# Kernel optimization log

Hardware: AMD Instinct MI355X
Metric: run time of the kernel (lower is better)

## Reference

```python
import jax, jax.numpy as jnp
import numpy as np

B, N, D_OBS, D_NB = 8192, 64, 128, 128
HEADS, GAT_F, GRU_H = 4, 64, 256
ACTION_DIM = 16
PERIOD0 = 24.0
NEG_SLOPE = 0.2
PMAX, PBUDGET = 0.5, 1.0
ENC_DIM = D_OBS + 1  # feature 0 expands to sin/cos
FUSE_IN = ENC_DIM + HEADS * GAT_F


def cyclical_encode(x):
    phase = 2.0 * jnp.pi * x[:, 0] / PERIOD0
    return jnp.concatenate([jnp.sin(phase)[:, None], jnp.cos(phase)[:, None], x[:, 1:]], axis=1)


def gat(node_feat, neigh_feat, mask, W, a):
    # node_feat [B,Din], neigh_feat [B,N,Din], W [Din,H*F], a [H,2F,1]
    b, n, _ = neigh_feat.shape
    h_node = (node_feat @ W).reshape(b, HEADS, GAT_F)            # [B,H,F]
    h_nb = (neigh_feat @ W).reshape(b, n, HEADS, GAT_F)          # [B,N,H,F]
    a_src, a_dst = a[:, :GAT_F, 0], a[:, GAT_F:, 0]              # [H,F] each
    e = (jnp.einsum('bhf,hf->bh', h_node, a_src)[:, None, :]
         + jnp.einsum('bnhf,hf->bnh', h_nb, a_dst))              # [B,N,H]
    e = jnp.where(e > 0, e, NEG_SLOPE * e)                        # leaky_relu
    e = jnp.where(mask[:, :, None], e, -jnp.inf)
    alpha = jax.nn.softmax(e, axis=1)                             # over neighbors
    agg = jnp.einsum('bnh,bnhf->bhf', alpha, h_nb)
    return agg.reshape(b, HEADS * GAT_F)


def gru_cell(x, h, Wih, bih, Whh, bhh):
    gi = x @ Wih + bih
    gh = h @ Whh + bhh
    ir, iz, in_ = jnp.split(gi, 3, axis=-1)
    hr, hz, hn = jnp.split(gh, 3, axis=-1)
    r = jax.nn.sigmoid(ir + hr)
    z = jax.nn.sigmoid(iz + hz)
    nn_ = jnp.tanh(in_ + r * hn)
    return (1.0 - z) * nn_ + z * h


def layer_norm(x, g, b, eps=1e-5):
    mu = jnp.mean(x, axis=-1, keepdims=True)
    var = jnp.var(x, axis=-1, keepdims=True)
    return (x - mu) * jax.lax.rsqrt(var + eps) * g + b


def project_power(raw):
    # Euclidean projection onto {0<=p<=PMAX, sum p<=PBUDGET} via bisection on mu
    def total(mu):
        return jnp.sum(jnp.clip(raw - mu[:, None], 0.0, PMAX), axis=1)
    feas = total(jnp.zeros(raw.shape[0], raw.dtype)) <= PBUDGET
    lo = jnp.zeros(raw.shape[0], raw.dtype)
    hi = jnp.maximum(jnp.max(raw, axis=1), 0.0)
    def body(_, lh):
        lo, hi = lh
        mid = 0.5 * (lo + hi)
        over = total(mid) > PBUDGET
        return (jnp.where(over, mid, lo), jnp.where(over, hi, mid))
    lo, hi = jax.lax.fori_loop(0, 60, body, (lo, hi))
    mu = jnp.where(feas, 0.0, hi)
    return jnp.clip(raw - mu[:, None], 0.0, PMAX)


def setup_inputs() -> dict:
    key = jax.random.key(0)
    ks = jax.random.split(key, 20)
    def init(k, shape, fan_in):
        return (jax.random.normal(k, shape, jnp.float32) / np.sqrt(fan_in)).astype(jnp.float32)
    mask = jax.random.bernoulli(ks[3], 0.5, (B, N))
    mask = mask.at[:, 0].set(True)  # guarantee >=1 valid neighbor per row
    return {
        'node_obs': jax.random.normal(ks[0], (B, D_OBS), jnp.float32),
        'neighbor_obs': jax.random.normal(ks[1], (B, N, D_NB), jnp.float32),
        'neighbor_mask': mask,
        'hidden_state': jnp.zeros((1, B, GRU_H), jnp.float32),
        'W_gat': init(ks[4], (D_NB, HEADS * GAT_F), D_NB),
        'a_gat': init(ks[5], (HEADS, 2 * GAT_F, 1), 2 * GAT_F),
        'fusion_W': init(ks[6], (FUSE_IN, GRU_H), FUSE_IN),
        'fusion_b': jnp.zeros((GRU_H,), jnp.float32),
        'Wih': init(ks[7], (GRU_H, 3 * GRU_H), GRU_H),
        'bih': jnp.zeros((3 * GRU_H,), jnp.float32),
        'Whh': init(ks[8], (GRU_H, 3 * GRU_H), GRU_H),
        'bhh': jnp.zeros((3 * GRU_H,), jnp.float32),
        'ln_g': jnp.ones((GRU_H,), jnp.float32),
        'ln_b': jnp.zeros((GRU_H,), jnp.float32),
        'W1': init(ks[9], (GRU_H, 256), GRU_H),
        'b1': jnp.zeros((256,), jnp.float32),
        'W2': init(ks[10], (256, 128), 256),
        'b2': jnp.zeros((128,), jnp.float32),
        'W3': init(ks[11], (128, ACTION_DIM), 128),
        'b3': jnp.zeros((ACTION_DIM,), jnp.float32),
    }


def reference(node_obs, neighbor_obs, neighbor_mask, hidden_state,
              W_gat, a_gat, fusion_W, fusion_b, Wih, bih, Whh, bhh,
              ln_g, ln_b, W1, b1, W2, b2, W3, b3):
    enc = cyclical_encode(node_obs)                              # [B, ENC_DIM]
    node_feat_for_gat = neighbor_obs[:, 0, :]
    ctx = gat(node_feat_for_gat, neighbor_obs, neighbor_mask, W_gat, a_gat)
    fused = jax.nn.relu(jnp.concatenate([enc, ctx], axis=-1) @ fusion_W + fusion_b)
    h_new = gru_cell(fused, hidden_state[0], Wih, bih, Whh, bhh)  # 1-step GRU
    belief = layer_norm(h_new, ln_g, ln_b)
    x = jax.nn.relu(belief @ W1 + b1)
    x = jax.nn.relu(x @ W2 + b2)
    raw = x @ W3 + b3                                            # [B, ACTION_DIM]
    action = project_power(raw)
    return action, h_new[None, :, :]
```

## Files before the change

kernel.cpp:

```cpp
#include <hip/hip_runtime.h>
#include <hip/hip_bf16.h>


typedef unsigned short u16;
typedef unsigned int   u32;
typedef __attribute__((ext_vector_type(8))) short bf16x8;
typedef __attribute__((ext_vector_type(4))) float f32x4;

#define KFUSE  672
#define ACT_TOT (8192*16)

__device__ __forceinline__ u16 f2bf(float x){
  u32 u = __float_as_uint(x);
  u += 0x7fffu + ((u >> 16) & 1u);
  return (u16)(u >> 16);
}
__device__ __forceinline__ float bf2f(u16 h){ return __uint_as_float(((u32)h) << 16); }

__device__ __forceinline__ void frag_one(const float* __restrict__ src, int ld, int col0,
                                         int NT, u16* __restrict__ dhi, u16* __restrict__ dlo,
                                         int f, int fsrc, int l){
  int kt = fsrc / NT, nt = fsrc % NT;
  int kbase = kt*32 + (l >> 4)*8, n = col0 + nt*16 + (l & 15);
  size_t o = ((size_t)f*64 + l)*8;
  #pragma unroll
  for(int i = 0; i < 8; ++i){
    float w = src[(size_t)(kbase + i)*ld + n];
    u16 h = f2bf(w);
    dhi[o + i] = h;
    dlo[o + i] = f2bf(w - bf2f(h));
  }
}

__device__ __forceinline__ void frag_wbig(const float* __restrict__ fW,
                                          const float* __restrict__ Wg,
                                          u16* __restrict__ dhi, u16* __restrict__ dlo,
                                          int f, int l){
  int kt = f / 16, nt = f % 16;
  int kbase = kt*32 + (l >> 4)*8, n = nt*16 + (l & 15);
  size_t o = ((size_t)f*64 + l)*8;
  #pragma unroll
  for(int i = 0; i < 8; ++i){
    int r = kbase + i;
    float v;
    if(r < 129) v = fW[(size_t)r*256 + n];
    else if(r < 641){
      int h = (r - 129) >> 7, kk = (r - 129) & 127;
      float s = 0.f;
      for(int ff = 0; ff < 64; ++ff)
        s += Wg[kk*256 + h*64 + ff] * fW[(size_t)(129 + h*64 + ff)*256 + n];
      v = s;
    } else v = 0.f;
    u16 hh = f2bf(v);
    dhi[o + i] = hh;
    dlo[o + i] = f2bf(v - bf2f(hh));
  }
}

#define P_FF0   1
#define P_WRZ0  85
#define P_WIN0  213
#define P_WHN0  245
#define P_F10   277
#define P_F20   309
__global__ __launch_bounds__(256) void k_prep(
    const unsigned char* __restrict__ maskb, int* __restrict__ flag,
    const float* __restrict__ Wg, const float* __restrict__ ag,
    float* __restrict__ was, float* __restrict__ wad,
    const float* __restrict__ fW,
    const float* __restrict__ Wih, const float* __restrict__ Whh,
    const float* __restrict__ W1, const float* __restrict__ W2,
    u16* __restrict__ ffh, u16* __restrict__ ffl,
    u16* __restrict__ wrzh, u16* __restrict__ wrzl,
    u16* __restrict__ winh, u16* __restrict__ winl,
    u16* __restrict__ whnh, u16* __restrict__ whnl,
    u16* __restrict__ f1h, u16* __restrict__ f1l,
    u16* __restrict__ f2h, u16* __restrict__ f2l)
{
  int bx = blockIdx.x, t = threadIdx.x;
  if(bx == 0){
    if(t == 0){
      int s = 0;
      for(int i = 1; i < 256; i += 4) s += maskb[i];
      *flag = (s == 0) ? 1 : 0;
    }
    #pragma unroll
    for(int v = 0; v < 2; ++v){
      int idx = v*256 + t, k = idx & 127, h = idx >> 7;
      float s = 0.f, d = 0.f;
      for(int f = 0; f < 64; ++f){
        float w = Wg[k*256 + h*64 + f];
        s += w * ag[h*128 + f];
        d += w * ag[h*128 + 64 + f];
      }
      was[k*4 + h] = s; wad[k*4 + h] = d;
    }
  } else if(bx < P_WRZ0){
    int sub = t >> 6, l = t & 63;
    int f = (bx - P_FF0)*4 + sub;
    frag_wbig(fW, Wg, ffh, ffl, f, l);
  } else {
    int sub = t >> 6, l = t & 63;
    if(bx < P_WIN0){
      int idx = (bx - P_WRZ0)*4 + sub;
      if(idx < 256) frag_one(Wih, 768, 0, 32, wrzh, wrzl, idx, idx, l);
      else          frag_one(Whh, 768, 0, 32, wrzh, wrzl, idx, idx - 256, l);
    } else if(bx < P_WHN0){
      int f = (bx - P_WIN0)*4 + sub;
      frag_one(Wih, 768, 512, 16, winh, winl, f, f, l);
    } else if(bx < P_F10){
      int f = (bx - P_WHN0)*4 + sub;
      frag_one(Whh, 768, 512, 16, whnh, whnl, f, f, l);
    } else if(bx < P_F20){
      int f = (bx - P_F10)*4 + sub;
      frag_one(W1, 256, 0, 16, f1h, f1l, f, f, l);
    } else {
      int f = (bx - P_F20)*4 + sub;
      frag_one(W2, 128, 0, 8, f2h, f2l, f, f, l);
    }
  }
}

__global__ __launch_bounds__(256) void k_gat(
    const float* __restrict__ nbg, const float* __restrict__ node,
    const void* __restrict__ maskp, const int* __restrict__ flagp,
    const float* __restrict__ was, const float* __restrict__ wad,
    u16* __restrict__ xhi, u16* __restrict__ xlo,
    const float* __restrict__ hidden,
    u16* __restrict__ acath, u16* __restrict__ acatl)
{
  int t = threadIdx.x;
  if(blockIdx.x >= 8192){
    int i = (blockIdx.x - 8192)*256 + t;
    int idx8 = i*8, row = idx8 >> 8, col = idx8 & 255;
    const float4* p = (const float4*)(hidden + (size_t)idx8);
    float4 v0 = p[0], v1 = p[1];
    float vv[8] = {v0.x,v0.y,v0.z,v0.w,v1.x,v1.y,v1.z,v1.w};
    u16 h8[8], l8[8];
    #pragma unroll
    for(int q = 0; q < 8; ++q){ u16 h = f2bf(vv[q]); h8[q] = h; l8[q] = f2bf(vv[q] - bf2f(h)); }
    uint4 uh = { (u32)h8[0] | ((u32)h8[1]<<16), (u32)h8[2] | ((u32)h8[3]<<16),
                 (u32)h8[4] | ((u32)h8[5]<<16), (u32)h8[6] | ((u32)h8[7]<<16) };
    uint4 ul = { (u32)l8[0] | ((u32)l8[1]<<16), (u32)l8[2] | ((u32)l8[3]<<16),
                 (u32)l8[4] | ((u32)l8[5]<<16), (u32)l8[6] | ((u32)l8[7]<<16) };
    size_t off = (size_t)row*512 + 256 + col;
    *(uint4*)(acath + off) = uh;
    *(uint4*)(acatl + off) = ul;
    return;
  }

  __shared__ float s_nb[8192];
  __shared__ float s_ep[1024];
  __shared__ float s_alpha[256];
  int b = blockIdx.x;
  const float* nb = nbg + (size_t)b*8192;
  const int isint = *flagp;

  #pragma unroll
  for(int q = 0; q < 8; ++q){
    int f = q*256 + t;
    int n = f >> 5, ch = f & 31;
    float4 v = *(const float4*)(nb + f*4);
    *(float4*)(s_nb + (n*32 + (ch ^ (n & 31)))*4) = v;
  }

  if(t < 129){
    float v;
    if(t < 2){
      float ph = node[(size_t)b*128] * (6.2831853071795864769f / 24.0f);
      v = (t == 0) ? sinf(ph) : cosf(ph);
    } else v = node[(size_t)b*128 + (t-1)];
    u16 h = f2bf(v);
    size_t o = (size_t)b*KFUSE + t;
    xhi[o] = h; xlo[o] = f2bf(v - bf2f(h));
  } else if(t < 160){
    size_t o = (size_t)b*KFUSE + 641 + (t - 129);
    xhi[o] = 0; xlo[o] = 0;
  }
  __syncthreads();

  {
    int n = t & 63, c = t >> 6;
    int cu = __builtin_amdgcn_readfirstlane(c);
    const float* wadc = wad + cu*128;
    float adx = 0.f, ady = 0.f, adz = 0.f, adw = 0.f;
    #pragma unroll
    for(int q = 0; q < 8; ++q){
      int ch = c*8 + q;
      float4 v = *(const float4*)(s_nb + (n*32 + (ch ^ (n & 31)))*4);
      float vv[4] = {v.x, v.y, v.z, v.w};
      #pragma unroll
      for(int i2 = 0; i2 < 4; ++i2){
        float4 wd = *(const float4*)(wadc + (q*4 + i2)*4);
        adx += vv[i2]*wd.x; ady += vv[i2]*wd.y; adz += vv[i2]*wd.z; adw += vv[i2]*wd.w;
      }
    }
    float4 ad = {adx, ady, adz, adw};
    *(float4*)(s_ep + (c*64 + n)*4) = ad;
  }
  __syncthreads();

  {
    int n2 = t & 63, h2 = t >> 6;
    float es = 0.f;
    #pragma unroll
    for(int ii = 0; ii < 2; ++ii){
      int k = n2*2 + ii;
      float v0 = s_nb[(k >> 2)*4 + (k & 3)];
      es += v0 * was[k*4 + h2];
    }
    for(int off = 32; off; off >>= 1) es += __shfl_xor(es, off);
    float ed = s_ep[n2*4 + h2] + s_ep[(64+n2)*4 + h2]
             + s_ep[(128+n2)*4 + h2] + s_ep[(192+n2)*4 + h2];
    float e = es + ed;
// ... 51 lines not shown
  }
}

template<int KT, int NT_TOT, int NPW, int ROWF>
__global__ __launch_bounds__(256) void k_gemm3(
    const u16* __restrict__ xhi, const u16* __restrict__ xlo, int lda,
    const u16* __restrict__ wfhi, const u16* __restrict__ wflo,
    const float* __restrict__ bias,
    u16* __restrict__ ohi, u16* __restrict__ olo, int ost, int ocol)
{
  int l = threadIdx.x & 63, w = threadIdx.x >> 6;
  int m0 = blockIdx.x * (16*ROWF);
  int ntbase = blockIdx.y * (4*NPW) + w*NPW;
  f32x4 acc[NPW][ROWF];
  #pragma unroll
  for(int j = 0; j < NPW; ++j)
    #pragma unroll
    for(int rf = 0; rf < ROWF; ++rf) acc[j][rf] = (f32x4){0.f,0.f,0.f,0.f};
  size_t arow[ROWF];
  #pragma unroll
  for(int rf = 0; rf < ROWF; ++rf)
    arow[rf] = (size_t)(m0 + rf*16 + (l & 15))*lda + (size_t)((l >> 4)*8);
  bf16x8 ah[ROWF], al[ROWF], bhc[NPW], blc[NPW];
  #pragma unroll
  for(int rf = 0; rf < ROWF; ++rf){
    ah[rf] = *(const bf16x8*)(xhi + arow[rf]);
    al[rf] = *(const bf16x8*)(xlo + arow[rf]);
  }
  #pragma unroll
  for(int j = 0; j < NPW; ++j){
    size_t bo = ((size_t)(ntbase + j)*64 + l)*8;
    bhc[j] = *(const bf16x8*)(wfhi + bo);
    blc[j] = *(const bf16x8*)(wflo + bo);
  }
  for(int kt = 0; kt < KT; ++kt){
    bf16x8 ahn[ROWF], aln[ROWF], bhn[NPW], bln[NPW];
    if(kt + 1 < KT){
      #pragma unroll
      for(int rf = 0; rf < ROWF; ++rf){
        ahn[rf] = *(const bf16x8*)(xhi + arow[rf] + (kt+1)*32);
        aln[rf] = *(const bf16x8*)(xlo + arow[rf] + (kt+1)*32);
      }
      #pragma unroll
      for(int j = 0; j < NPW; ++j){
        size_t bo = ((size_t)((kt+1)*NT_TOT + ntbase + j)*64 + l)*8;
        bhn[j] = *(const bf16x8*)(wfhi + bo);
        bln[j] = *(const bf16x8*)(wflo + bo);
      }
    }
    #pragma unroll
    for(int j = 0; j < NPW; ++j){
      #pragma unroll
      for(int rf = 0; rf < ROWF; ++rf){
        acc[j][rf] = __builtin_amdgcn_mfma_f32_16x16x32_bf16(ah[rf], bhc[j], acc[j][rf], 0, 0, 0);
        acc[j][rf] = __builtin_amdgcn_mfma_f32_16x16x32_bf16(ah[rf], blc[j], acc[j][rf], 0, 0, 0);
        acc[j][rf] = __builtin_amdgcn_mfma_f32_16x16x32_bf16(al[rf], bhc[j], acc[j][rf], 0, 0, 0);
      }
    }
    #pragma unroll
    for(int rf = 0; rf < ROWF; ++rf){ ah[rf] = ahn[rf]; al[rf] = aln[rf]; }
    #pragma unroll
    for(int j = 0; j < NPW; ++j){ bhc[j] = bhn[j]; blc[j] = bln[j]; }
  }
  #pragma unroll
  for(int j = 0; j < NPW; ++j){
    int col = (ntbase + j)*16 + (l & 15);
    float bv = bias[col];
    #pragma unroll
    for(int rf = 0; rf < ROWF; ++rf){
      int r0 = m0 + rf*16 + (l >> 4)*4;
      #pragma unroll
      for(int q = 0; q < 4; ++q){
        float y = fmaxf(acc[j][rf][q] + bv, 0.f);
        size_t o = (size_t)(r0 + q)*ost + ocol + col;
        u16 h = f2bf(y);
        ohi[o] = h; olo[o] = f2bf(y - bf2f(h));
      }
    }
  }
}

#define BSTR 264
#define XSTR 132
__global__ __launch_bounds__(512) void k_grumlp(
    const u16* __restrict__ ah_, const u16* __restrict__ al_,
    const u16* __restrict__ wrzh, const u16* __restrict__ wrzl,
    const u16* __restrict__ winh, const u16* __restrict__ winl,
    const u16* __restrict__ whnh, const u16* __restrict__ whnl,
    const u16* __restrict__ f1h, const u16* __restrict__ f1l,
    const u16* __restrict__ f2h, const u16* __restrict__ f2l,
    const float* __restrict__ bih, const float* __restrict__ bhh,
    const float* __restrict__ hidden, const float* __restrict__ lng,
    const float* __restrict__ lnb,
    const float* __restrict__ b1, const float* __restrict__ b2,
    const float* __restrict__ W3, const float* __restrict__ b3,
    float* __restrict__ hout, float* __restrict__ act)
{
  __shared__ float s_s1[256], s_s2[256], s_mu[32], s_rs[32];
  __shared__ u16 s_bh[32*BSTR], s_bl[32*BSTR];
  __shared__ float s_x2[32*XSTR];
  __shared__ float sW3[2048];
  int t = threadIdx.x;
  int l = t & 63, w = t >> 6;
  int m0 = blockIdx.x*32;
  for(int i = t; i < 2048; i += 512) sW3[i] = W3[i];

  f32x4 ar[2][2], az[2][2], aa[2][2], ab[2][2];
  #pragma unroll
  for(int j = 0; j < 2; ++j)
    #pragma unroll
    for(int rf = 0; rf < 2; ++rf){
      ar[j][rf] = (f32x4){0.f,0.f,0.f,0.f}; az[j][rf] = (f32x4){0.f,0.f,0.f,0.f};
      aa[j][rf] = (f32x4){0.f,0.f,0.f,0.f}; ab[j][rf] = (f32x4){0.f,0.f,0.f,0.f};
    }
  size_t arow[2];
  #pragma unroll
  for(int rf = 0; rf < 2; ++rf)
    arow[rf] = (size_t)(m0 + rf*16 + (l & 15))*512 + (size_t)((l >> 4)*8);
  for(int kt = 0; kt < 16; ++kt){
    bf16x8 xh[2], xl[2];
    #pragma unroll
    for(int rf = 0; rf < 2; ++rf){
      xh[rf] = *(const bf16x8*)(ah_ + arow[rf] + kt*32);
      xl[rf] = *(const bf16x8*)(al_ + arow[rf] + kt*32);
    }
    #pragma unroll
    for(int j = 0; j < 2; ++j){
      int nt = w*2 + j;
      size_t bo = ((size_t)(kt*32 + nt)*64 + l)*8;
      bf16x8 bh = *(const bf16x8*)(wrzh + bo);
      bf16x8 bl = *(const bf16x8*)(wrzl + bo);
      size_t bo2 = bo + (size_t)16*64*8;
      bf16x8 bh2 = *(const bf16x8*)(wrzh + bo2);
      bf16x8 bl2 = *(const bf16x8*)(wrzl + bo2);
      #pragma unroll
      for(int rf = 0; rf < 2; ++rf){
        ar[j][rf] = __builtin_amdgcn_mfma_f32_16x16x32_bf16(xh[rf], bh, ar[j][rf], 0, 0, 0);
        ar[j][rf] = __builtin_amdgcn_mfma_f32_16x16x32_bf16(xh[rf], bl, ar[j][rf], 0, 0, 0);
        ar[j][rf] = __builtin_amdgcn_mfma_f32_16x16x32_bf16(xl[rf], bh, ar[j][rf], 0, 0, 0);
        az[j][rf] = __builtin_amdgcn_mfma_f32_16x16x32_bf16(xh[rf], bh2, az[j][rf], 0, 0, 0);
        az[j][rf] = __builtin_amdgcn_mfma_f32_16x16x32_bf16(xh[rf], bl2, az[j][rf], 0, 0, 0);
        az[j][rf] = __builtin_amdgcn_mfma_f32_16x16x32_bf16(xl[rf], bh2, az[j][rf], 0, 0, 0);
      }
    }
  }
  for(int kt = 0; kt < 8; ++kt){
    bf16x8 fh[2], fl2[2], gh[2], gl[2];
    #pragma unroll
    for(int rf = 0; rf < 2; ++rf){
      fh[rf]  = *(const bf16x8*)(ah_ + arow[rf] + kt*32);
      fl2[rf] = *(const bf16x8*)(al_ + arow[rf] + kt*32);
      gh[rf]  = *(const bf16x8*)(ah_ + arow[rf] + 256 + kt*32);
      gl[rf]  = *(const bf16x8*)(al_ + arow[rf] + 256 + kt*32);
    }
    #pragma unroll
    for(int j = 0; j < 2; ++j){
      int nt = w*2 + j;
      size_t bo = ((size_t)(kt*16 + nt)*64 + l)*8;
      bf16x8 bh = *(const bf16x8*)(winh + bo);
      bf16x8 bl = *(const bf16x8*)(winl + bo);
      bf16x8 ch = *(const bf16x8*)(whnh + bo);
      bf16x8 cl2 = *(const bf16x8*)(whnl + bo);
      #pragma unroll
      for(int rf = 0; rf < 2; ++rf){
        aa[j][rf] = __builtin_amdgcn_mfma_f32_16x16x32_bf16(fh[rf], bh, aa[j][rf], 0, 0, 0);
        aa[j][rf] = __builtin_amdgcn_mfma_f32_16x16x32_bf16(fh[rf], bl, aa[j][rf], 0, 0, 0);
        aa[j][rf] = __builtin_amdgcn_mfma_f32_16x16x32_bf16(fl2[rf], bh, aa[j][rf], 0, 0, 0);
        ab[j][rf] = __builtin_amdgcn_mfma_f32_16x16x32_bf16(gh[rf], ch, ab[j][rf], 0, 0, 0);
        ab[j][rf] = __builtin_amdgcn_mfma_f32_16x16x32_bf16(gh[rf], cl2, ab[j][rf], 0, 0, 0);
        ab[j][rf] = __builtin_amdgcn_mfma_f32_16x16x32_bf16(gl[rf], ch, ab[j][rf], 0, 0, 0);
      }
    }
  }
  int cl = l & 15, rq = l >> 4;
  float hnew[2][2][4];
  float s1p[2][4], s2p[2][4];
  #pragma unroll
  for(int rf = 0; rf < 2; ++rf)
    #pragma unroll
    for(int q = 0; q < 4; ++q){ s1p[rf][q] = 0.f; s2p[rf][q] = 0.f; }
  #pragma unroll
  for(int j = 0; j < 2; ++j){
    int col = w*32 + j*16 + cl;
    float br = bih[col] + bhh[col];
    float bz = bih[256+col] + bhh[256+col];
    float bi = bih[512+col];
    float bh2 = bhh[512+col];
    #pragma unroll
    for(int rf = 0; rf < 2; ++rf){
      #pragma unroll
      for(int q = 0; q < 4; ++q){
        int row = m0 + rf*16 + rq*4 + q;
        float rs = ar[j][rf][q] + br;
        float zs = az[j][rf][q] + bz;
        float in_ = aa[j][rf][q] + bi;
        float hn  = ab[j][rf][q] + bh2;
        float h   = hidden[(size_t)row*256 + col];
        float r = 1.f/(1.f + expf(-rs));
        float z = 1.f/(1.f + expf(-zs));
        float nv = tanhf(in_ + r*hn);
        float hv = (1.f - z)*nv + z*h;
        hnew[j][rf][q] = hv;
        hout[(size_t)row*256 + col] = hv;
        s1p[rf][q] += hv; s2p[rf][q] += hv*hv;
      }
    }
  }
  #pragma unroll
  for(int rf = 0; rf < 2; ++rf)
    #pragma unroll
    for(int q = 0; q < 4; ++q){
      float a = s1p[rf][q], b2v = s2p[rf][q];
      for(int off = 1; off < 16; off <<= 1){
        a += __shfl_xor(a, off); b2v += __shfl_xor(b2v, off);
      }
      if(cl == 0){
        int rloc = rf*16 + rq*4 + q;
        s_s1[w*32 + rloc] = a; s_s2[w*32 + rloc] = b2v;
      }
    }
  __syncthreads();
  if(t < 32){
    int rloc = t;
    float t1 = 0.f, t2 = 0.f;
    #pragma unroll
    for(int ww = 0; ww < 8; ++ww){ t1 += s_s1[ww*32 + rloc]; t2 += s_s2[ww*32 + rloc]; }
    float mu = t1 * (1.f/256.f);
    float var = t2 * (1.f/256.f) - mu*mu;
    s_mu[rloc] = mu; s_rs[rloc] = rsqrtf(var + 1e-5f);
  }
  __syncthreads();
  #pragma unroll
  for(int j = 0; j < 2; ++j){
    int col = w*32 + j*16 + cl;
    float g = lng[col], bb = lnb[col];
    #pragma unroll
    for(int rf = 0; rf < 2; ++rf){
      #pragma unroll
      for(int q = 0; q < 4; ++q){
        int rloc = rf*16 + rq*4 + q;
        float bel = (hnew[j][rf][q] - s_mu[rloc]) * s_rs[rloc] * g + bb;
        u16 hb = f2bf(bel);
        s_bh[rloc*BSTR + col] = hb;
        s_bl[rloc*BSTR + col] = f2bf(bel - bf2f(hb));
      }
    }
  }
  __syncthreads();
  f32x4 ax1[2][2];
  #pragma unroll
  for(int j = 0; j < 2; ++j)
    #pragma unroll
    for(int rf = 0; rf < 2; ++rf) ax1[j][rf] = (f32x4){0.f,0.f,0.f,0.f};
  for(int kt = 0; kt < 8; ++kt){
    bf16x8 xh[2], xl[2];
    #pragma unroll
    for(int rf = 0; rf < 2; ++rf){
      int off = (rf*16 + (l & 15))*BSTR + kt*32 + (l >> 4)*8;
      xh[rf] = *(const bf16x8*)(s_bh + off);
      xl[rf] = *(const bf16x8*)(s_bl + off);
    }
    #pragma unroll
    for(int j = 0; j < 2; ++j){
      size_t bo = ((size_t)(kt*16 + w*2 + j)*64 + l)*8;
      bf16x8 bh = *(const bf16x8*)(f1h + bo);
      bf16x8 bl = *(const bf16x8*)(f1l + bo);
      #pragma unroll
      for(int rf = 0; rf < 2; ++rf){
        ax1[j][rf] = __builtin_amdgcn_mfma_f32_16x16x32_bf16(xh[rf], bh, ax1[j][rf], 0, 0, 0);
        ax1[j][rf] = __builtin_amdgcn_mfma_f32_16x16x32_bf16(xh[rf], bl, ax1[j][rf], 0, 0, 0);
        ax1[j][rf] = __builtin_amdgcn_mfma_f32_16x16x32_bf16(xl[rf], bh, ax1[j][rf], 0, 0, 0);
      }
    }
  }
  __syncthreads();
  #pragma unroll
  for(int j = 0; j < 2; ++j){
    int col = (w*2 + j)*16 + cl;
    float bv = b1[col];
    #pragma unroll
    for(int rf = 0; rf < 2; ++rf){
      #pragma unroll
      for(int q = 0; q < 4; ++q){
        int rloc = rf*16 + rq*4 + q;
        float y = fmaxf(ax1[j][rf][q] + bv, 0.f);
        u16 hh = f2bf(y);
        s_bh[rloc*BSTR + col] = hh;
        s_bl[rloc*BSTR + col] = f2bf(y - bf2f(hh));
      }
    }
  }
  __syncthreads();
  f32x4 ax2[2];
  #pragma unroll
  for(int rf = 0; rf < 2; ++rf) ax2[rf] = (f32x4){0.f,0.f,0.f,0.f};
  for(int kt = 0; kt < 8; ++kt){
    bf16x8 xh[2], xl[2];
    #pragma unroll
    for(int rf = 0; rf < 2; ++rf){
      int off = (rf*16 + (l & 15))*BSTR + kt*32 + (l >> 4)*8;
      xh[rf] = *(const bf16x8*)(s_bh + off);
      xl[rf] = *(const bf16x8*)(s_bl + off);
    }
    size_t bo = ((size_t)(kt*8 + w)*64 + l)*8;
    bf16x8 bh = *(const bf16x8*)(f2h + bo);
    bf16x8 bl = *(const bf16x8*)(f2l + bo);
    #pragma unroll
    for(int rf = 0; rf < 2; ++rf){
      ax2[rf] = __builtin_amdgcn_mfma_f32_16x16x32_bf16(xh[rf], bh, ax2[rf], 0, 0, 0);
      ax2[rf] = __builtin_amdgcn_mfma_f32_16x16x32_bf16(xh[rf], bl, ax2[rf], 0, 0, 0);
      ax2[rf] = __builtin_amdgcn_mfma_f32_16x16x32_bf16(xl[rf], bh, ax2[rf], 0, 0, 0);
    }
  }
  {
    int col = w*16 + cl;
    float bv = b2[col];
    #pragma unroll
    for(int rf = 0; rf < 2; ++rf)
      #pragma unroll
      for(int q = 0; q < 4; ++q){
        int rloc = rf*16 + rq*4 + q;
        s_x2[rloc*XSTR + col] = fmaxf(ax2[rf][q] + bv, 0.f);
      }
  }
  __syncthreads();
  {
    int j = t & 15, rl = t >> 4;
    const float* xr = s_x2 + rl*XSTR;
    float raw = b3[j];
    #pragma unroll 8
    for(int k4 = 0; k4 < 32; ++k4){
      float4 v = *(const float4*)(xr + k4*4);
      raw += v.x*sW3[(k4*4+0)*16 + j] + v.y*sW3[(k4*4+1)*16 + j]
           + v.z*sW3[(k4*4+2)*16 + j] + v.w*sW3[(k4*4+3)*16 + j];
    }
    float c0 = fminf(fmaxf(raw, 0.f), 0.5f);
    float tot = c0;
    for(int off = 8; off; off >>= 1) tot += __shfl_xor(tot, off);
    float mx = raw;
    for(int off = 8; off; off >>= 1) mx = fmaxf(mx, __shfl_xor(mx, off));
    bool feas = (tot <= 1.0f);
    float lo = 0.f, hi = fmaxf(mx, 0.f);
    for(int it = 0; it < 60; ++it){
      float mid = 0.5f*(lo + hi);
      float s = fminf(fmaxf(raw - mid, 0.f), 0.5f);
      for(int off = 8; off; off >>= 1) s += __shfl_xor(s, off);
      bool over = s > 1.0f;
      lo = over ? mid : lo;
      hi = over ? hi : mid;
    }
    float muv = feas ? 0.f : hi;
    act[(size_t)(m0 + rl)*16 + j] = fminf(fmaxf(raw - muv, 0.f), 0.5f);
  }
}

#define OFF_FLAG   0u
#define OFF_WAS    4096u
#define OFF_WAD    8192u
#define OFF_FFH    12288u
#define OFF_FFL    356352u
#define OFF_WRZH   700416u
#define OFF_WRZL   1224704u
#define OFF_WINH   1748992u
#define OFF_WINL   1880064u
#define OFF_WHNH   2011136u
#define OFF_WHNL   2142208u
#define OFF_F1H    2273280u
#define OFF_F1L    2404352u
#define OFF_F2H    2535424u
#define OFF_F2L    2600960u
#define OFF_XCATH  2666496u
#define OFF_XCATL  13676544u
#define OFF_ACATH  24686592u
#define OFF_ACATL  33075200u

extern "C" void kernel_launch(void* const* d_in, const int* in_sizes, int n_in,
                              void* d_out, int out_size, void* d_ws, size_t ws_size,
                              hipStream_t stream){
  const float* node   = (const float*)d_in[0];
  const float* nbr    = (const float*)d_in[1];
  const void*  mask   = d_in[2];
  const float* hidden = (const float*)d_in[3];
  const float* Wg     = (const float*)d_in[4];
  const float* ag     = (const float*)d_in[5];
  const float* fW     = (const float*)d_in[6];
  const float* fb     = (const float*)d_in[7];
  const float* Wih    = (const float*)d_in[8];
  const float* bih    = (const float*)d_in[9];
  const float* Whh    = (const float*)d_in[10];
  const float* bhh    = (const float*)d_in[11];
  const float* lng    = (const float*)d_in[12];
  const float* lnb    = (const float*)d_in[13];
  const float* W1     = (const float*)d_in[14];
  const float* b1     = (const float*)d_in[15];
  const float* W2     = (const float*)d_in[16];
  const float* b2     = (const float*)d_in[17];
  const float* W3     = (const float*)d_in[18];
  const float* b3     = (const float*)d_in[19];
  char* ws = (char*)d_ws;
  float* out = (float*)d_out;

  int*   flag = (int*)  (ws + OFF_FLAG);
  float* was  = (float*)(ws + OFF_WAS);
  float* wad  = (float*)(ws + OFF_WAD);
  u16* ffh  = (u16*)(ws + OFF_FFH);   u16* ffl  = (u16*)(ws + OFF_FFL);
  u16* wrzh = (u16*)(ws + OFF_WRZH);  u16* wrzl = (u16*)(ws + OFF_WRZL);
  u16* winh = (u16*)(ws + OFF_WINH);  u16* winl = (u16*)(ws + OFF_WINL);
  u16* whnh = (u16*)(ws + OFF_WHNH);  u16* whnl = (u16*)(ws + OFF_WHNL);
  u16* f1h  = (u16*)(ws + OFF_F1H);   u16* f1l  = (u16*)(ws + OFF_F1L);
  u16* f2h  = (u16*)(ws + OFF_F2H);   u16* f2l  = (u16*)(ws + OFF_F2L);
  u16* xh   = (u16*)(ws + OFF_XCATH); u16* xl   = (u16*)(ws + OFF_XCATL);
  u16* ach  = (u16*)(ws + OFF_ACATH); u16* acl  = (u16*)(ws + OFF_ACATL);

  k_prep<<<325, 256, 0, stream>>>((const unsigned char*)mask, flag, Wg, ag, was, wad,
                                  fW, Wih, Whh, W1, W2,
                                  ffh, ffl, wrzh, wrzl, winh, winl, whnh, whnl,
                                  f1h, f1l, f2h, f2l);

  k_gat<<<8192 + 1024, 256, 0, stream>>>(nbr, node, mask, flag, was, wad, xh, xl,
                                         hidden, ach, acl);

  k_gemm3<21,16,2,4><<<dim3(128,2), 256, 0, stream>>>(xh, xl, KFUSE, ffh, ffl, fb, ach, acl, 512, 0);

  k_grumlp<<<256, 512, 0, stream>>>(ach, acl, wrzh, wrzl, winh, winl, whnh, whnl,
                                    f1h, f1l, f2h, f2l, bih, bhh, hidden, lng, lnb,
                                    b1, b2, W3, b3, out + ACT_TOT, out);
}
```

Measured before the change: 178.6 us.

## Move fused-weight prep into GAT kernel and double-buffer GRU GEMM loads

Moves the expensive frag_wbig work, which builds the combined GAT and fusion weight fragments, out of k_prep and into 84 extra blocks of k_gat. That work then overlaps with the GAT blocks instead of delaying the start of k_gat, and k_prep shrinks from 325 to 241 blocks. Separately, the GRU GEMM loops in k_grumlp now prefetch the next k-step's A and B fragments into registers while MFMAs run on the current ones, which raises register pressure. The frag_wbig blocks sit at the highest block indices, so they may be scheduled last and lengthen k_gat's tail.

```diff
diff --git a/kernel.cpp b/kernel.cpp
--- a/kernel.cpp
+++ b/kernel.cpp
@@ -57,20 +57,17 @@
   }
 }
 
-#define P_FF0   1
-#define P_WRZ0  85
-#define P_WIN0  213
-#define P_WHN0  245
-#define P_F10   277
-#define P_F20   309
+#define P_WRZ0  1
+#define P_WIN0  129
+#define P_WHN0  161
+#define P_F10   193
+#define P_F20   225
 __global__ __launch_bounds__(256) void k_prep(
     const unsigned char* __restrict__ maskb, int* __restrict__ flag,
     const float* __restrict__ Wg, const float* __restrict__ ag,
     float* __restrict__ was, float* __restrict__ wad,
-    const float* __restrict__ fW,
     const float* __restrict__ Wih, const float* __restrict__ Whh,
     const float* __restrict__ W1, const float* __restrict__ W2,
-    u16* __restrict__ ffh, u16* __restrict__ ffl,
     u16* __restrict__ wrzh, u16* __restrict__ wrzl,
     u16* __restrict__ winh, u16* __restrict__ winl,
     u16* __restrict__ whnh, u16* __restrict__ whnl,
@@ -95,10 +92,6 @@
       }
       was[k*4 + h] = s; wad[k*4 + h] = d;
     }
-  } else if(bx < P_WRZ0){
-    int sub = t >> 6, l = t & 63;
-    int f = (bx - P_FF0)*4 + sub;
-    frag_wbig(fW, Wg, ffh, ffl, f, l);
   } else {
     int sub = t >> 6, l = t & 63;
     if(bx < P_WIN0){
@@ -127,9 +120,16 @@
     const float* __restrict__ was, const float* __restrict__ wad,
     u16* __restrict__ xhi, u16* __restrict__ xlo,
     const float* __restrict__ hidden,
-    u16* __restrict__ acath, u16* __restrict__ acatl)
+    u16* __restrict__ acath, u16* __restrict__ acatl,
+    const float* __restrict__ fW, const float* __restrict__ Wg,
+    u16* __restrict__ ffh, u16* __restrict__ ffl)
 {
   int t = threadIdx.x;
+  if(blockIdx.x >= 9216){
+    int f = (blockIdx.x - 9216)*4 + (t >> 6), l = t & 63;
+    frag_wbig(fW, Wg, ffh, ffl, f, l);
+    return;
+  }
   if(blockIdx.x >= 8192){
     int i = (blockIdx.x - 8192)*256 + t;
     int idx8 = i*8, row = idx8 >> 8, col = idx8 & 255;
@@ -382,58 +382,113 @@
   #pragma unroll
   for(int rf = 0; rf < 2; ++rf)
     arow[rf] = (size_t)(m0 + rf*16 + (l & 15))*512 + (size_t)((l >> 4)*8);
-  for(int kt = 0; kt < 16; ++kt){
-    bf16x8 xh[2], xl[2];
-    #pragma unroll
-    for(int rf = 0; rf < 2; ++rf){
-      xh[rf] = *(const bf16x8*)(ah_ + arow[rf] + kt*32);
-      xl[rf] = *(const bf16x8*)(al_ + arow[rf] + kt*32);
+  {
+    bf16x8 xhc[2], xlc[2], bhc[2], blc[2], bh2c[2], bl2c[2];
+    #pragma unroll
+    for(int rf = 0; rf < 2; ++rf){
+      xhc[rf] = *(const bf16x8*)(ah_ + arow[rf]);
+      xlc[rf] = *(const bf16x8*)(al_ + arow[rf]);
     }
     #pragma unroll
     for(int j = 0; j < 2; ++j){
-      int nt = w*2 + j;
-      size_t bo = ((size_t)(kt*32 + nt)*64 + l)*8;
-      bf16x8 bh = *(const bf16x8*)(wrzh + bo);
-      bf16x8 bl = *(const bf16x8*)(wrzl + bo);
-      size_t bo2 = bo + (size_t)16*64*8;
-      bf16x8 bh2 = *(const bf16x8*)(wrzh + bo2);
-      bf16x8 bl2 = *(const bf16x8*)(wrzl + bo2);
+      size_t bo = ((size_t)(w*2 + j)*64 + l)*8;
+      bhc[j]  = *(const bf16x8*)(wrzh + bo);
+      blc[j]  = *(const bf16x8*)(wrzl + bo);
+      bh2c[j] = *(const bf16x8*)(wrzh + bo + (size_t)16*64*8);
+      bl2c[j] = *(const bf16x8*)(wrzl + bo + (size_t)16*64*8);
+    }
+    for(int kt = 0; kt < 16; ++kt){
+      bf16x8 xhn[2], xln[2], bhn[2], bln[2], bh2n[2], bl2n[2];
+      if(kt + 1 < 16){
+        #pragma unroll
+        for(int rf = 0; rf < 2; ++rf){
+          xhn[rf] = *(const bf16x8*)(ah_ + arow[rf] + (kt+1)*32);
+          xln[rf] = *(const bf16x8*)(al_ + arow[rf] + (kt+1)*32);
+        }
+        #pragma unroll
+        for(int j = 0; j < 2; ++j){
+          size_t bo = ((size_t)((kt+1)*32 + w*2 + j)*64 + l)*8;
+          bhn[j]  = *(const bf16x8*)(wrzh + bo);
+          bln[j]  = *(const bf16x8*)(wrzl + bo);
+          bh2n[j] = *(const bf16x8*)(wrzh + bo + (size_t)16*64*8);
+          bl2n[j] = *(const bf16x8*)(wrzl + bo + (size_t)16*64*8);
+        }
+      }
+      #pragma unroll
+      for(int j = 0; j < 2; ++j){
+        #pragma unroll
+        for(int rf = 0; rf < 2; ++rf){
+          ar[j][rf] = __builtin_amdgcn_mfma_f32_16x16x32_bf16(xhc[rf], bhc[j], ar[j][rf], 0, 0, 0);
+          ar[j][rf] = __builtin_amdgcn_mfma_f32_16x16x32_bf16(xhc[rf], blc[j], ar[j][rf], 0, 0, 0);
+          ar[j][rf] = __builtin_amdgcn_mfma_f32_16x16x32_bf16(xlc[rf], bhc[j], ar[j][rf], 0, 0, 0);
+          az[j][rf] = __builtin_amdgcn_mfma_f32_16x16x32_bf16(xhc[rf], bh2c[j], az[j][rf], 0, 0, 0);
+          az[j][rf] = __builtin_amdgcn_mfma_f32_16x16x32_bf16(xhc[rf], bl2c[j], az[j][rf], 0, 0, 0);
+          az[j][rf] = __builtin_amdgcn_mfma_f32_16x16x32_bf16(xlc[rf], bh2c[j], az[j][rf], 0, 0, 0);
+        }
+      }
+      #pragma unroll
+      for(int rf = 0; rf < 2; ++rf){ xhc[rf] = xhn[rf]; xlc[rf] = xln[rf]; }
+      #pragma unroll
+      for(int j = 0; j < 2; ++j){
+        bhc[j] = bhn[j]; blc[j] = bln[j]; bh2c[j] = bh2n[j]; bl2c[j] = bl2n[j];
+      }
+    }
+  }
+  {
+    bf16x8 fhc[2], flc[2], ghc[2], glc[2], bhc[2], blc[2], chc[2], clc[2];
+    #pragma unroll
+    for(int rf = 0; rf < 2; ++rf){
+      fhc[rf] = *(const bf16x8*)(ah_ + arow[rf]);
+      flc[rf] = *(const bf16x8*)(al_ + arow[rf]);
+      ghc[rf] = *(const bf16x8*)(ah_ + arow[rf] + 256);
+      glc[rf] = *(const bf16x8*)(al_ + arow[rf] + 256);
+    }
+    #pragma unroll
+    for(int j = 0; j < 2; ++j){
+      size_t bo = ((size_t)(w*2 + j)*64 + l)*8;
+      bhc[j] = *(const bf16x8*)(winh + bo);
+      blc[j] = *(const bf16x8*)(winl + bo);
+      chc[j] = *(const bf16x8*)(whnh + bo);
+      clc[j] = *(const bf16x8*)(whnl + bo);
+    }
+    for(int kt = 0; kt < 8; ++kt){
+      bf16x8 fhn[2], fln[2], ghn[2], gln[2], bhn[2], bln[2], chn[2], cln[2];
+      if(kt + 1 < 8){
+        #pragma unroll
+        for(int rf = 0; rf < 2; ++rf){
+          fhn[rf] = *(const bf16x8*)(ah_ + arow[rf] + (kt+1)*32);
+          fln[rf] = *(const bf16x8*)(al_ + arow[rf] + (kt+1)*32);
+          ghn[rf] = *(const bf16x8*)(ah_ + arow[rf] + 256 + (kt+1)*32);
+          gln[rf] = *(const bf16x8*)(al_ + arow[rf] + 256 + (kt+1)*32);
+        }
+        #pragma unroll
+        for(int j = 0; j < 2; ++j){
+          size_t bo = ((size_t)((kt+1)*16 + w*2 + j)*64 + l)*8;
+          bhn[j] = *(const bf16x8*)(winh + bo);
+          bln[j] = *(const bf16x8*)(winl + bo);
+          chn[j] = *(const bf16x8*)(whnh + bo);
+          cln[j] = *(const bf16x8*)(whnl + bo);
+        }
+      }
+      #pragma unroll
+      for(int j = 0; j < 2; ++j){
+        #pragma unroll
+        for(int rf = 0; rf < 2; ++rf){
+          aa[j][rf] = __builtin_amdgcn_mfma_f32_16x16x32_bf16(fhc[rf], bhc[j], aa[j][rf], 0, 0, 0);
+          aa[j][rf] = __builtin_amdgcn_mfma_f32_16x16x32_bf16(fhc[rf], blc[j], aa[j][rf], 0, 0, 0);
+          aa[j][rf] = __builtin_amdgcn_mfma_f32_16x16x32_bf16(flc[rf], bhc[j], aa[j][rf], 0, 0, 0);
+          ab[j][rf] = __builtin_amdgcn_mfma_f32_16x16x32_bf16(ghc[rf], chc[j], ab[j][rf], 0, 0, 0);
+          ab[j][rf] = __builtin_amdgcn_mfma_f32_16x16x32_bf16(ghc[rf], clc[j], ab[j][rf], 0, 0, 0);
+          ab[j][rf] = __builtin_amdgcn_mfma_f32_16x16x32_bf16(glc[rf], chc[j], ab[j][rf], 0, 0, 0);
+        }
+      }
       #pragma unroll
       for(int rf = 0; rf < 2; ++rf){
-        ar[j][rf] = __builtin_amdgcn_mfma_f32_16x16x32_bf16(xh[rf], bh, ar[j][rf], 0, 0, 0);
-        ar[j][rf] = __builtin_amdgcn_mfma_f32_16x16x32_bf16(xh[rf], bl, ar[j][rf], 0, 0, 0);
-        ar[j][rf] = __builtin_amdgcn_mfma_f32_16x16x32_bf16(xl[rf], bh, ar[j][rf], 0, 0, 0);
-        az[j][rf] = __builtin_amdgcn_mfma_f32_16x16x32_bf16(xh[rf], bh2, az[j][rf], 0, 0, 0);
-        az[j][rf] = __builtin_amdgcn_mfma_f32_16x16x32_bf16(xh[rf], bl2, az[j][rf], 0, 0, 0);
-        az[j][rf] = __builtin_amdgcn_mfma_f32_16x16x32_bf16(xl[rf], bh2, az[j][rf], 0, 0, 0);
-      }
-    }
-  }
-  for(int kt = 0; kt < 8; ++kt){
-    bf16x8 fh[2], fl2[2], gh[2], gl[2];
-    #pragma unroll
-    for(int rf = 0; rf < 2; ++rf){
-      fh[rf]  = *(const bf16x8*)(ah_ + arow[rf] + kt*32);
-      fl2[rf] = *(const bf16x8*)(al_ + arow[rf] + kt*32);
-      gh[rf]  = *(const bf16x8*)(ah_ + arow[rf] + 256 + kt*32);
-      gl[rf]  = *(const bf16x8*)(al_ + arow[rf] + 256 + kt*32);
-    }
-    #pragma unroll
-    for(int j = 0; j < 2; ++j){
-      int nt = w*2 + j;
-      size_t bo = ((size_t)(kt*16 + nt)*64 + l)*8;
-      bf16x8 bh = *(const bf16x8*)(winh + bo);
-      bf16x8 bl = *(const bf16x8*)(winl + bo);
-      bf16x8 ch = *(const bf16x8*)(whnh + bo);
-      bf16x8 cl2 = *(const bf16x8*)(whnl + bo);
-      #pragma unroll
-      for(int rf = 0; rf < 2; ++rf){
-        aa[j][rf] = __builtin_amdgcn_mfma_f32_16x16x32_bf16(fh[rf], bh, aa[j][rf], 0, 0, 0);
-        aa[j][rf] = __builtin_amdgcn_mfma_f32_16x16x32_bf16(fh[rf], bl, aa[j][rf], 0, 0, 0);
-        aa[j][rf] = __builtin_amdgcn_mfma_f32_16x16x32_bf16(fl2[rf], bh, aa[j][rf], 0, 0, 0);
-        ab[j][rf] = __builtin_amdgcn_mfma_f32_16x16x32_bf16(gh[rf], ch, ab[j][rf], 0, 0, 0);
-        ab[j][rf] = __builtin_amdgcn_mfma_f32_16x16x32_bf16(gh[rf], cl2, ab[j][rf], 0, 0, 0);
-        ab[j][rf] = __builtin_amdgcn_mfma_f32_16x16x32_bf16(gl[rf], ch, ab[j][rf], 0, 0, 0);
+        fhc[rf] = fhn[rf]; flc[rf] = fln[rf]; ghc[rf] = ghn[rf]; glc[rf] = gln[rf];
+      }
+      #pragma unroll
+      for(int j = 0; j < 2; ++j){
+        bhc[j] = bhn[j]; blc[j] = bln[j]; chc[j] = chn[j]; clc[j] = cln[j];
       }
     }
   }
@@ -677,13 +732,13 @@
   u16* xh   = (u16*)(ws + OFF_XCATH); u16* xl   = (u16*)(ws + OFF_XCATL);
   u16* ach  = (u16*)(ws + OFF_ACATH); u16* acl  = (u16*)(ws + OFF_ACATL);
 
-  k_prep<<<325, 256, 0, stream>>>((const unsigned char*)mask, flag, Wg, ag, was, wad,
-                                  fW, Wih, Whh, W1, W2,
-                                  ffh, ffl, wrzh, wrzl, winh, winl, whnh, whnl,
+  k_prep<<<241, 256, 0, stream>>>((const unsigned char*)mask, flag, Wg, ag, was, wad,
+                                  Wih, Whh, W1, W2,
+                                  wrzh, wrzl, winh, winl, whnh, whnl,
                                   f1h, f1l, f2h, f2l);
 
-  k_gat<<<8192 + 1024, 256, 0, stream>>>(nbr, node, mask, flag, was, wad, xh, xl,
-                                         hidden, ach, acl);
+  k_gat<<<8192 + 1024 + 84, 256, 0, stream>>>(nbr, node, mask, flag, was, wad, xh, xl,
+                                              hidden, ach, acl, fW, Wg, ffh, ffl);
 
   k_gemm3<21,16,2,4><<<dim3(128,2), 256, 0, stream>>>(xh, xl, KFUSE, ffh, ffl, fb, ach, acl, 512, 0);
 
```

Result: no change. 182.0 us (+1.9%).

## Double waves per block in GRU/MLP kernel and shrink fusion GEMM tiles

Applied to the files above, without the earlier changes.

The GRU+MLP kernel now runs 1024 threads per block, and each wave owns one 16-column tile instead of two. This halves the accumulator registers per wave and doubles the waves available to hide MFMA and load latency. The LayerNorm partial-sum reduction is widened to 16 waves. Only 8 waves do the second MLP layer and only half the threads do the projection. The fusion GEMM launch switches to smaller tile parameters with a 256x4 grid, which gives more blocks to fill the CUs. The cost is more idle waves in the later stages and extra block-level synchronisation overhead.

```diff
diff --git a/kernel.cpp b/kernel.cpp
--- a/kernel.cpp
+++ b/kernel.cpp
@@ -347,7 +347,7 @@
 
 #define BSTR 264
 #define XSTR 132
-__global__ __launch_bounds__(512) void k_grumlp(
+__global__ __launch_bounds__(1024) void k_grumlp(
     const u16* __restrict__ ah_, const u16* __restrict__ al_,
     const u16* __restrict__ wrzh, const u16* __restrict__ wrzl,
     const u16* __restrict__ winh, const u16* __restrict__ winl,
@@ -361,23 +361,21 @@
     const float* __restrict__ W3, const float* __restrict__ b3,
     float* __restrict__ hout, float* __restrict__ act)
 {
-  __shared__ float s_s1[256], s_s2[256], s_mu[32], s_rs[32];
+  __shared__ float s_s1[512], s_s2[512], s_mu[32], s_rs[32];
   __shared__ u16 s_bh[32*BSTR], s_bl[32*BSTR];
   __shared__ float s_x2[32*XSTR];
   __shared__ float sW3[2048];
   int t = threadIdx.x;
   int l = t & 63, w = t >> 6;
   int m0 = blockIdx.x*32;
-  for(int i = t; i < 2048; i += 512) sW3[i] = W3[i];
-
-  f32x4 ar[2][2], az[2][2], aa[2][2], ab[2][2];
-  #pragma unroll
-  for(int j = 0; j < 2; ++j)
-    #pragma unroll
-    for(int rf = 0; rf < 2; ++rf){
-      ar[j][rf] = (f32x4){0.f,0.f,0.f,0.f}; az[j][rf] = (f32x4){0.f,0.f,0.f,0.f};
-      aa[j][rf] = (f32x4){0.f,0.f,0.f,0.f}; ab[j][rf] = (f32x4){0.f,0.f,0.f,0.f};
-    }
+  for(int i = t; i < 2048; i += 1024) sW3[i] = W3[i];
+
+  f32x4 ar[2], az[2], aa[2], ab[2];
+  #pragma unroll
+  for(int rf = 0; rf < 2; ++rf){
+    ar[rf] = (f32x4){0.f,0.f,0.f,0.f}; az[rf] = (f32x4){0.f,0.f,0.f,0.f};
+    aa[rf] = (f32x4){0.f,0.f,0.f,0.f}; ab[rf] = (f32x4){0.f,0.f,0.f,0.f};
+  }
   size_t arow[2];
   #pragma unroll
   for(int rf = 0; rf < 2; ++rf)
@@ -389,24 +387,20 @@
       xh[rf] = *(const bf16x8*)(ah_ + arow[rf] + kt*32);
       xl[rf] = *(const bf16x8*)(al_ + arow[rf] + kt*32);
     }
-    #pragma unroll
-    for(int j = 0; j < 2; ++j){
-      int nt = w*2 + j;
-      size_t bo = ((size_t)(kt*32 + nt)*64 + l)*8;
-      bf16x8 bh = *(const bf16x8*)(wrzh + bo);
-      bf16x8 bl = *(const bf16x8*)(wrzl + bo);
-      size_t bo2 = bo + (size_t)16*64*8;
-      bf16x8 bh2 = *(const bf16x8*)(wrzh + bo2);
-      bf16x8 bl2 = *(const bf16x8*)(wrzl + bo2);
-      #pragma unroll
-      for(int rf = 0; rf < 2; ++rf){
-        ar[j][rf] = __builtin_amdgcn_mfma_f32_16x16x32_bf16(xh[rf], bh, ar[j][rf], 0, 0, 0);
-        ar[j][rf] = __builtin_amdgcn_mfma_f32_16x16x32_bf16(xh[rf], bl, ar[j][rf], 0, 0, 0);
-        ar[j][rf] = __builtin_amdgcn_mfma_f32_16x16x32_bf16(xl[rf], bh, ar[j][rf], 0, 0, 0);
-        az[j][rf] = __builtin_amdgcn_mfma_f32_16x16x32_bf16(xh[rf], bh2, az[j][rf], 0, 0, 0);
-        az[j][rf] = __builtin_amdgcn_mfma_f32_16x16x32_bf16(xh[rf], bl2, az[j][rf], 0, 0, 0);
-        az[j][rf] = __builtin_amdgcn_mfma_f32_16x16x32_bf16(xl[rf], bh2, az[j][rf], 0, 0, 0);
-      }
+    size_t bo = ((size_t)(kt*32 + w)*64 + l)*8;
+    bf16x8 bh = *(const bf16x8*)(wrzh + bo);
+    bf16x8 bl = *(const bf16x8*)(wrzl + bo);
+    size_t bo2 = bo + (size_t)16*64*8;
+    bf16x8 bh2 = *(const bf16x8*)(wrzh + bo2);
+    bf16x8 bl2 = *(const bf16x8*)(wrzl + bo2);
+    #pragma unroll
+    for(int rf = 0; rf < 2; ++rf){
+      ar[rf] = __builtin_amdgcn_mfma_f32_16x16x32_bf16(xh[rf], bh, ar[rf], 0, 0, 0);
+      ar[rf] = __builtin_amdgcn_mfma_f32_16x16x32_bf16(xh[rf], bl, ar[rf], 0, 0, 0);
+      ar[rf] = __builtin_amdgcn_mfma_f32_16x16x32_bf16(xl[rf], bh, ar[rf], 0, 0, 0);
+      az[rf] = __builtin_amdgcn_mfma_f32_16x16x32_bf16(xh[rf], bh2, az[rf], 0, 0, 0);
+      az[rf] = __builtin_amdgcn_mfma_f32_16x16x32_bf16(xh[rf], bl2, az[rf], 0, 0, 0);
+      az[rf] = __builtin_amdgcn_mfma_f32_16x16x32_bf16(xl[rf], bh2, az[rf], 0, 0, 0);
     }
   }
   for(int kt = 0; kt < 8; ++kt){
@@ -418,35 +412,26 @@
       gh[rf]  = *(const bf16x8*)(ah_ + arow[rf] + 256 + kt*32);
       gl[rf]  = *(const bf16x8*)(al_ + arow[rf] + 256 + kt*32);
     }
-    #pragma unroll
-    for(int j = 0; j < 2; ++j){
-      int nt = w*2 + j;
-      size_t bo = ((size_t)(kt*16 + nt)*64 + l)*8;
-      bf16x8 bh = *(const bf16x8*)(winh + bo);
-      bf16x8 bl = *(const bf16x8*)(winl + bo);
-      bf16x8 ch = *(const bf16x8*)(whnh + bo);
-      bf16x8 cl2 = *(const bf16x8*)(whnl + bo);
-      #pragma unroll
-      for(int rf = 0; rf < 2; ++rf){
-        aa[j][rf] = __builtin_amdgcn_mfma_f32_16x16x32_bf16(fh[rf], bh, aa[j][rf], 0, 0, 0);
-        aa[j][rf] = __builtin_amdgcn_mfma_f32_16x16x32_bf16(fh[rf], bl, aa[j][rf], 0, 0, 0);
-        aa[j][rf] = __builtin_amdgcn_mfma_f32_16x16x32_bf16(fl2[rf], bh, aa[j][rf], 0, 0, 0);
-        ab[j][rf] = __builtin_amdgcn_mfma_f32_16x16x32_bf16(gh[rf], ch, ab[j][rf], 0, 0, 0);
-        ab[j][rf] = __builtin_amdgcn_mfma_f32_16x16x32_bf16(gh[rf], cl2, ab[j][rf], 0, 0, 0);
-        ab[j][rf] = __builtin_amdgcn_mfma_f32_16x16x32_bf16(gl[rf], ch, ab[j][rf], 0, 0, 0);
-      }
+    size_t bo = ((size_t)(kt*16 + w)*64 + l)*8;
+    bf16x8 bh = *(const bf16x8*)(winh + bo);
+    bf16x8 bl = *(const bf16x8*)(winl + bo);
+    bf16x8 ch = *(const bf16x8*)(whnh + bo);
+    bf16x8 cl2 = *(const bf16x8*)(whnl + bo);
+    #pragma unroll
+    for(int rf = 0; rf < 2; ++rf){
+      aa[rf] = __builtin_amdgcn_mfma_f32_16x16x32_bf16(fh[rf], bh, aa[rf], 0, 0, 0);
+      aa[rf] = __builtin_amdgcn_mfma_f32_16x16x32_bf16(fh[rf], bl, aa[rf], 0, 0, 0);
+      aa[rf] = __builtin_amdgcn_mfma_f32_16x16x32_bf16(fl2[rf], bh, aa[rf], 0, 0, 0);
+      ab[rf] = __builtin_amdgcn_mfma_f32_16x16x32_bf16(gh[rf], ch, ab[rf], 0, 0, 0);
+      ab[rf] = __builtin_amdgcn_mfma_f32_16x16x32_bf16(gh[rf], cl2, ab[rf], 0, 0, 0);
+      ab[rf] = __builtin_amdgcn_mfma_f32_16x16x32_bf16(gl[rf], ch, ab[rf], 0, 0, 0);
     }
   }
   int cl = l & 15, rq = l >> 4;
-  float hnew[2][2][4];
+  float hnew[2][4];
   float s1p[2][4], s2p[2][4];
-  #pragma unroll
-  for(int rf = 0; rf < 2; ++rf)
-    #pragma unroll
-    for(int q = 0; q < 4; ++q){ s1p[rf][q] = 0.f; s2p[rf][q] = 0.f; }
-  #pragma unroll
-  for(int j = 0; j < 2; ++j){
-    int col = w*32 + j*16 + cl;
+  {
+    int col = w*16 + cl;
     float br = bih[col] + bhh[col];
     float bz = bih[256+col] + bhh[256+col];
     float bi = bih[512+col];
@@ -456,18 +441,18 @@
       #pragma unroll
       for(int q = 0; q < 4; ++q){
         int row = m0 + rf*16 + rq*4 + q;
-        float rs = ar[j][rf][q] + br;
-        float zs = az[j][rf][q] + bz;
-        float in_ = aa[j][rf][q] + bi;
-        float hn  = ab[j][rf][q] + bh2;
+        float rs = ar[rf][q] + br;
+        float zs = az[rf][q] + bz;
+        float in_ = aa[rf][q] + bi;
+        float hn  = ab[rf][q] + bh2;
         float h   = hidden[(size_t)row*256 + col];
         float r = 1.f/(1.f + expf(-rs));
         float z = 1.f/(1.f + expf(-zs));
         float nv = tanhf(in_ + r*hn);
         float hv = (1.f - z)*nv + z*h;
-        hnew[j][rf][q] = hv;
+        hnew[rf][q] = hv;
         hout[(size_t)row*256 + col] = hv;
-        s1p[rf][q] += hv; s2p[rf][q] += hv*hv;
+        s1p[rf][q] = hv; s2p[rf][q] = hv*hv;
       }
     }
   }
@@ -489,22 +474,21 @@
     int rloc = t;
     float t1 = 0.f, t2 = 0.f;
     #pragma unroll
-    for(int ww = 0; ww < 8; ++ww){ t1 += s_s1[ww*32 + rloc]; t2 += s_s2[ww*32 + rloc]; }
+    for(int ww = 0; ww < 16; ++ww){ t1 += s_s1[ww*32 + rloc]; t2 += s_s2[ww*32 + rloc]; }
     float mu = t1 * (1.f/256.f);
     float var = t2 * (1.f/256.f) - mu*mu;
     s_mu[rloc] = mu; s_rs[rloc] = rsqrtf(var + 1e-5f);
   }
   __syncthreads();
-  #pragma unroll
-  for(int j = 0; j < 2; ++j){
-    int col = w*32 + j*16 + cl;
+  {
+    int col = w*16 + cl;
     float g = lng[col], bb = lnb[col];
     #pragma unroll
     for(int rf = 0; rf < 2; ++rf){
       #pragma unroll
       for(int q = 0; q < 4; ++q){
         int rloc = rf*16 + rq*4 + q;
-        float bel = (hnew[j][rf][q] - s_mu[rloc]) * s_rs[rloc] * g + bb;
+        float bel = (hnew[rf][q] - s_mu[rloc]) * s_rs[rloc] * g + bb;
         u16 hb = f2bf(bel);
         s_bh[rloc*BSTR + col] = hb;
         s_bl[rloc*BSTR + col] = f2bf(bel - bf2f(hb));
@@ -512,11 +496,9 @@
     }
   }
   __syncthreads();
-  f32x4 ax1[2][2];
-  #pragma unroll
-  for(int j = 0; j < 2; ++j)
-    #pragma unroll
-    for(int rf = 0; rf < 2; ++rf) ax1[j][rf] = (f32x4){0.f,0.f,0.f,0.f};
+  f32x4 ax1[2];
+  #pragma unroll
+  for(int rf = 0; rf < 2; ++rf) ax1[rf] = (f32x4){0.f,0.f,0.f,0.f};
   for(int kt = 0; kt < 8; ++kt){
     bf16x8 xh[2], xl[2];
     #pragma unroll
@@ -525,30 +507,26 @@
       xh[rf] = *(const bf16x8*)(s_bh + off);
       xl[rf] = *(const bf16x8*)(s_bl + off);
     }
-    #pragma unroll
-    for(int j = 0; j < 2; ++j){
-      size_t bo = ((size_t)(kt*16 + w*2 + j)*64 + l)*8;
-      bf16x8 bh = *(const bf16x8*)(f1h + bo);
-      bf16x8 bl = *(const bf16x8*)(f1l + bo);
-      #pragma unroll
-      for(int rf = 0; rf < 2; ++rf){
-        ax1[j][rf] = __builtin_amdgcn_mfma_f32_16x16x32_bf16(xh[rf], bh, ax1[j][rf], 0, 0, 0);
-        ax1[j][rf] = __builtin_amdgcn_mfma_f32_16x16x32_bf16(xh[rf], bl, ax1[j][rf], 0, 0, 0);
-        ax1[j][rf] = __builtin_amdgcn_mfma_f32_16x16x32_bf16(xl[rf], bh, ax1[j][rf], 0, 0, 0);
-      }
-    }
-  }
-  __syncthreads();
-  #pragma unroll
-  for(int j = 0; j < 2; ++j){
-    int col = (w*2 + j)*16 + cl;
+    size_t bo = ((size_t)(kt*16 + w)*64 + l)*8;
+    bf16x8 bh = *(const bf16x8*)(f1h + bo);
+    bf16x8 bl = *(const bf16x8*)(f1l + bo);
+    #pragma unroll
+    for(int rf = 0; rf < 2; ++rf){
+      ax1[rf] = __builtin_amdgcn_mfma_f32_16x16x32_bf16(xh[rf], bh, ax1[rf], 0, 0, 0);
+      ax1[rf] = __builtin_amdgcn_mfma_f32_16x16x32_bf16(xh[rf], bl, ax1[rf], 0, 0, 0);
+      ax1[rf] = __builtin_amdgcn_mfma_f32_16x16x32_bf16(xl[rf], bh, ax1[rf], 0, 0, 0);
+    }
+  }
+  __syncthreads();
+  {
+    int col = w*16 + cl;
     float bv = b1[col];
     #pragma unroll
     for(int rf = 0; rf < 2; ++rf){
       #pragma unroll
       for(int q = 0; q < 4; ++q){
         int rloc = rf*16 + rq*4 + q;
-        float y = fmaxf(ax1[j][rf][q] + bv, 0.f);
+        float y = fmaxf(ax1[rf][q] + bv, 0.f);
         u16 hh = f2bf(y);
         s_bh[rloc*BSTR + col] = hh;
         s_bl[rloc*BSTR + col] = f2bf(y - bf2f(hh));
@@ -556,28 +534,28 @@
     }
   }
   __syncthreads();
-  f32x4 ax2[2];
-  #pragma unroll
-  for(int rf = 0; rf < 2; ++rf) ax2[rf] = (f32x4){0.f,0.f,0.f,0.f};
-  for(int kt = 0; kt < 8; ++kt){
-    bf16x8 xh[2], xl[2];
-    #pragma unroll
-    for(int rf = 0; rf < 2; ++rf){
-      int off = (rf*16 + (l & 15))*BSTR + kt*32 + (l >> 4)*8;
-      xh[rf] = *(const bf16x8*)(s_bh + off);
-      xl[rf] = *(const bf16x8*)(s_bl + off);
-    }
-    size_t bo = ((size_t)(kt*8 + w)*64 + l)*8;
-    bf16x8 bh = *(const bf16x8*)(f2h + bo);
-    bf16x8 bl = *(const bf16x8*)(f2l + bo);
-    #pragma unroll
-    for(int rf = 0; rf < 2; ++rf){
-      ax2[rf] = __builtin_amdgcn_mfma_f32_16x16x32_bf16(xh[rf], bh, ax2[rf], 0, 0, 0);
-      ax2[rf] = __builtin_amdgcn_mfma_f32_16x16x32_bf16(xh[rf], bl, ax2[rf], 0, 0, 0);
-      ax2[rf] = __builtin_amdgcn_mfma_f32_16x16x32_bf16(xl[rf], bh, ax2[rf], 0, 0, 0);
-    }
-  }
-  {
+  if(w < 8){
+    f32x4 ax2[2];
+    #pragma unroll
+    for(int rf = 0; rf < 2; ++rf) ax2[rf] = (f32x4){0.f,0.f,0.f,0.f};
+    for(int kt = 0; kt < 8; ++kt){
+      bf16x8 xh[2], xl[2];
+      #pragma unroll
+      for(int rf = 0; rf < 2; ++rf){
+        int off = (rf*16 + (l & 15))*BSTR + kt*32 + (l >> 4)*8;
+        xh[rf] = *(const bf16x8*)(s_bh + off);
+        xl[rf] = *(const bf16x8*)(s_bl + off);
+      }
+      size_t bo = ((size_t)(kt*8 + w)*64 + l)*8;
+      bf16x8 bh = *(const bf16x8*)(f2h + bo);
+      bf16x8 bl = *(const bf16x8*)(f2l + bo);
+      #pragma unroll
+      for(int rf = 0; rf < 2; ++rf){
+        ax2[rf] = __builtin_amdgcn_mfma_f32_16x16x32_bf16(xh[rf], bh, ax2[rf], 0, 0, 0);
+        ax2[rf] = __builtin_amdgcn_mfma_f32_16x16x32_bf16(xh[rf], bl, ax2[rf], 0, 0, 0);
+        ax2[rf] = __builtin_amdgcn_mfma_f32_16x16x32_bf16(xl[rf], bh, ax2[rf], 0, 0, 0);
+      }
+    }
     int col = w*16 + cl;
     float bv = b2[col];
     #pragma unroll
@@ -589,7 +567,7 @@
       }
   }
   __syncthreads();
-  {
+  if(t < 512){
     int j = t & 15, rl = t >> 4;
     const float* xr = s_x2 + rl*XSTR;
     float raw = b3[j];
@@ -685,9 +663,9 @@
   k_gat<<<8192 + 1024, 256, 0, stream>>>(nbr, node, mask, flag, was, wad, xh, xl,
                                          hidden, ach, acl);
 
-  k_gemm3<21,16,2,4><<<dim3(128,2), 256, 0, stream>>>(xh, xl, KFUSE, ffh, ffl, fb, ach, acl, 512, 0);
-
-  k_grumlp<<<256, 512, 0, stream>>>(ach, acl, wrzh, wrzl, winh, winl, whnh, whnl,
-                                    f1h, f1l, f2h, f2l, bih, bhh, hidden, lng, lnb,
-                                    b1, b2, W3, b3, out + ACT_TOT, out);
-}
+  k_gemm3<21,16,1,2><<<dim3(256,4), 256, 0, stream>>>(xh, xl, KFUSE, ffh, ffl, fb, ach, acl, 512, 0);
+
+  k_grumlp<<<256, 1024, 0, stream>>>(ach, acl, wrzh, wrzl, winh, winl, whnh, whnl,
+                                     f1h, f1l, f2h, f2l, bih, bhh, hidden, lng, lnb,
+                                     b1, b2, W3, b3, out + ACT_TOT, out);
+}
```

After: 206.0 us. +15.3%, slower.
